# Kernel tuning notes

Measured on AMD Instinct MI355X. Metric: run time of the kernel, lower is better.

Reference implementation:

```python
import jax, jax.numpy as jnp
import numpy as np

CUTOFF = 4          # lattice cutoff radius (module init arg)
NMAX = 64           # padded max neighbors per mobile site (~58 actual at cutoff=4)
BATCH = 131072      # number of independent configurations
B_SOFT = 0.01       # softening constant b in vint
FAR = 1e6           # padding position, masked out


def _rot(c):
    return np.array([[np.cos(c), -np.sin(c)], [np.sin(c), np.cos(c)]])


def _build_geometry():
    """Replicates PotEnergy1P.__init__ (with the intended, bug-fixed math)."""
    s3 = np.sqrt(3.0)
    base = [np.array([0.5, s3 / 6]), np.array([1.0, -s3 / 3]),
            np.array([1.5, s3 / 6]), np.array([1.0, 2 * s3 / 3])]
    mobile = base \
        + [_rot(2 * np.pi / 3) @ p for p in base] \
        + [_rot(4 * np.pi / 3) @ p for p in base]
    mobile = np.stack(mobile)                      # [12, 2]

    def ntopos(n1, n2):
        return np.array([0.5, s3 / 6]) + n1 * np.array([1.0, 0.0]) \
            + n2 * np.array([-0.5, s3 / 2])

    rng = range(-4 * CUTOFF, 4 * CUTOFF)
    grid = np.array([ntopos(n1, n2) for n1 in rng for n2 in rng])  # [G, 2]
    dist = np.linalg.norm(grid[:, None, :] - mobile[None, :, :], axis=-1)  # [G, 12]
    not_mobile = ~np.any(np.isclose(dist, 0.0, atol=1e-8), axis=1)        # [G]

    neighbors = np.full((12, NMAX, 2), FAR, dtype=np.float32)
    mask = np.zeros((12, NMAX), dtype=np.float32)
    for i in range(12):
        idx = np.where(not_mobile & (dist[:, i] < CUTOFF))[0]
        k = len(idx)
        assert k <= NMAX
        neighbors[i, :k] = grid[idx]
        mask[i, :k] = 1.0
    return neighbors, mask


def setup_inputs() -> dict:
    key = jax.random.key(0)
    x = jax.random.normal(key, (BATCH, 24), dtype=jnp.float32)
    neighbors, mask = _build_geometry()
    return {"x": x,
            "neighbors": jnp.asarray(neighbors),
            "mask": jnp.asarray(mask)}


def reference(x, neighbors, mask):
    # x: [B, 24] -> [B, 12, 2] mobile positions
    xr = x.reshape(x.shape[0], -1, 2)
    # pairwise displacement to all padded neighbors: [B, 12, NMAX, 2]
    d = xr[:, :, None, :] - neighbors[None, :, :, :]
    r = jnp.sqrt(jnp.sum(d * d, axis=-1))          # [B, 12, NMAX]
    v = jnp.exp(-r) / (r + B_SOFT)                 # vint with a=1.0, b=0.01
    return jnp.sum(v * mask[None], axis=(1, 2))    # [B] total potential energy
```

## Files before the change

### kernel.cpp

```cpp
#include <hip/hip_runtime.h>

#define NMAX   64
#define NSITES 12
#define SPLIT  2
#define BLOCK  256

__global__ __launch_bounds__(BLOCK, 4)
void pot_energy_kernel(const float* __restrict__ x,
                       const float* __restrict__ neighbors,
                       float* __restrict__ out, int B) {
    __shared__ float2 nb[NSITES * 65];

    const int tid = threadIdx.x;
    for (int idx = tid; idx < NSITES * NMAX; idx += BLOCK) {
        const int i = idx >> 6;
        const int j = idx & 63;
        nb[i * 65 + j] = ((const float2*)neighbors)[idx];
    }
    __syncthreads();

    const int gtid = blockIdx.x * BLOCK + tid;
    const int e = gtid >> 1;
    const int h = gtid & 1;
    if (e >= B) return;

    const float4* xp = (const float4*)(x + (size_t)gtid * 12);
    const float4 a0 = xp[0], a1 = xp[1], a2 = xp[2];
    const float xs_[6] = { a0.x, a0.z, a1.x, a1.z, a2.x, a2.z };
    const float ys_[6] = { a0.y, a0.w, a1.y, a1.w, a2.y, a2.w };

    float acc0 = 0.f, acc1 = 0.f;
    #pragma unroll
    for (int s = 0; s < 6; ++s) {
        const float xs = xs_[s];
        const float ys = ys_[s];
        const float2* __restrict__ row = &nb[(h * 6 + s) * 65];
        #pragma unroll 8
        for (int j = 0; j < NMAX; ++j) {
            const float2 n = row[j];
            const float dx = xs - n.x;
            const float dy = ys - n.y;
            const float r2 = fmaf(dy, dy, dx * dx);
            const float r  = __builtin_amdgcn_sqrtf(r2);
            const float ex = __expf(-r);
            const float rc = __builtin_amdgcn_rcpf(r + 0.01f);
            if (j & 1) acc1 = fmaf(ex, rc, acc1);
            else       acc0 = fmaf(ex, rc, acc0);
        }
    }

    float total = acc0 + acc1;
    total += __shfl_xor(total, 1);
    if (h == 0) out[e] = total;
}

extern "C" void kernel_launch(void* const* d_in, const int* in_sizes, int n_in,
                              void* d_out, int out_size, void* d_ws, size_t ws_size,
                              hipStream_t stream) {
    const float* x   = (const float*)d_in[0];
    const float* nbr = (const float*)d_in[1];
    float* out = (float*)d_out;

    const int B = in_sizes[0] / 24;
    const int total_threads = B * SPLIT;
    const int blocks = (total_threads + BLOCK - 1) / BLOCK;
    pot_energy_kernel<<<blocks, BLOCK, 0, stream>>>(x, nbr, out, B);
}
```

Measured before the change: 96.99 us.

## Compact masked neighbors, loop only to max count, fold log2e scaling, split 4 ways

```diff
diff --git a/kernel.cpp b/kernel.cpp
--- a/kernel.cpp
+++ b/kernel.cpp
@@ -2,56 +2,81 @@
 
 #define NMAX   64
 #define NSITES 12
-#define SPLIT  2
+#define SPLIT  4
 #define BLOCK  256
+#define ROWS   66
 
-__global__ __launch_bounds__(BLOCK, 4)
+#define LOG2E  1.44269504088896340736f
+#define LN2    0.69314718055994530942f
+#define B_SOFT 0.01f
+#define PAD_C  2.0e6f
+
+__global__ __launch_bounds__(BLOCK, 8)
 void pot_energy_kernel(const float* __restrict__ x,
                        const float* __restrict__ neighbors,
+                       const float* __restrict__ mask,
                        float* __restrict__ out, int B) {
-    __shared__ float2 nb[NSITES * 65];
+    __shared__ float2 nb[NSITES * ROWS];
+    __shared__ int    cnt[NSITES];
 
-    const int tid = threadIdx.x;
-    for (int idx = tid; idx < NSITES * NMAX; idx += BLOCK) {
-        const int i = idx >> 6;
-        const int j = idx & 63;
-        nb[i * 65 + j] = ((const float2*)neighbors)[idx];
+    const int tid  = threadIdx.x;
+    const int wv   = tid >> 6;
+    const int lane = tid & 63;
+
+    for (int idx = tid; idx < NSITES * ROWS; idx += BLOCK)
+        nb[idx] = make_float2(PAD_C, PAD_C);
+    __syncthreads();
+
+    for (int s = wv; s < NSITES; s += 4) {
+        const bool keep = mask[s * NMAX + lane] > 0.5f;
+        const unsigned long long bal = __ballot(keep);
+        if (keep) {
+            const int pos = __popcll(bal & ((1ull << lane) - 1ull));
+            const float2 p = ((const float2*)neighbors)[s * NMAX + lane];
+            nb[s * ROWS + pos] = make_float2(p.x * LOG2E, p.y * LOG2E);
+        }
+        if (lane == 0) cnt[s] = __popcll(bal);
     }
     __syncthreads();
 
+    int m = 0;
+    #pragma unroll
+    for (int s = 0; s < NSITES; ++s) m = max(m, cnt[s]);
+    m = __builtin_amdgcn_readfirstlane(m);
+
     const int gtid = blockIdx.x * BLOCK + tid;
-    const int e = gtid >> 1;
-    const int h = gtid & 1;
+    const int e = gtid >> 2;
+    const int q = gtid & 3;
     if (e >= B) return;
 
-    const float4* xp = (const float4*)(x + (size_t)gtid * 12);
-    const float4 a0 = xp[0], a1 = xp[1], a2 = xp[2];
-    const float xs_[6] = { a0.x, a0.z, a1.x, a1.z, a2.x, a2.z };
-    const float ys_[6] = { a0.y, a0.w, a1.y, a1.w, a2.y, a2.w };
+    const float2* xp = (const float2*)(x + (size_t)gtid * 6);
+    const float2 p0 = xp[0], p1 = xp[1], p2 = xp[2];
+    const float xs_[3] = { p0.x * LOG2E, p1.x * LOG2E, p2.x * LOG2E };
+    const float ys_[3] = { p0.y * LOG2E, p1.y * LOG2E, p2.y * LOG2E };
 
-    float acc0 = 0.f, acc1 = 0.f;
+    float acc = 0.f;
     #pragma unroll
-    for (int s = 0; s < 6; ++s) {
+    for (int s = 0; s < 3; ++s) {
+        const int site = q * 3 + s;
         const float xs = xs_[s];
         const float ys = ys_[s];
-        const float2* __restrict__ row = &nb[(h * 6 + s) * 65];
+        const float2* __restrict__ row = &nb[site * ROWS];
         #pragma unroll 8
-        for (int j = 0; j < NMAX; ++j) {
-            const float2 n = row[j];
-            const float dx = xs - n.x;
-            const float dy = ys - n.y;
+        for (int j = 0; j < m; ++j) {
+            const float2 nj = row[j];
+            const float dx = xs - nj.x;
+            const float dy = ys - nj.y;
             const float r2 = fmaf(dy, dy, dx * dx);
-            const float r  = __builtin_amdgcn_sqrtf(r2);
-            const float ex = __expf(-r);
-            const float rc = __builtin_amdgcn_rcpf(r + 0.01f);
-            if (j & 1) acc1 = fmaf(ex, rc, acc1);
-            else       acc0 = fmaf(ex, rc, acc0);
+            const float rp = __builtin_amdgcn_sqrtf(r2);
+            const float ex = __builtin_amdgcn_exp2f(-rp);
+            const float dn = fmaf(rp, LN2, B_SOFT);
+            acc = fmaf(ex, __builtin_amdgcn_rcpf(dn), acc);
         }
     }
 
-    float total = acc0 + acc1;
-    total += __shfl_xor(total, 1);
-    if (h == 0) out[e] = total;
+    acc += __shfl_xor(acc, 1);
+    acc += __shfl_xor(acc, 2);
+    if (q == 0) out[e] = acc;
 }
 
 extern "C" void kernel_launch(void* const* d_in, const int* in_sizes, int n_in,
@@ -59,10 +84,11 @@
                               hipStream_t stream) {
     const float* x   = (const float*)d_in[0];
     const float* nbr = (const float*)d_in[1];
+    const float* msk = (const float*)d_in[2];
     float* out = (float*)d_out;
 
     const int B = in_sizes[0] / 24;
     const int total_threads = B * SPLIT;
     const int blocks = (total_threads + BLOCK - 1) / BLOCK;
-    pot_energy_kernel<<<blocks, BLOCK, 0, stream>>>(x, nbr, out, B);
+    pot_energy_kernel<<<blocks, BLOCK, 0, stream>>>(x, nbr, msk, out, B);
 }
```

Result: faster. 86.76 us (-10.5%).
